# Performance work log

Hardware: AMD Instinct MI355X
Metric: run time of the kernel (lower is better)

## Reference

```python
import jax, jax.numpy as jnp
import numpy as np

S, B, C = 7, 2, 20
L_OBJ, L_NOBJ = 5.0, 0.5
EPS = 1e-06


def setup_inputs() -> dict:
    key = jax.random.key(0)
    k1, k2, k3 = jax.random.split(key, 3)
    N = 16384
    pred = jax.random.normal(k1, (N, S, S, B * 5 + C), dtype=jnp.float32)
    tgt = jax.random.uniform(k2, (N, S, S, 5 + C), dtype=jnp.float32)
    # objectness flag must be exactly 0.0 or 1.0 (loss tests true_box[0] == 1)
    obj = (jax.random.uniform(k3, (N, S, S)) < 0.3).astype(jnp.float32)
    target = tgt.at[..., 0].set(obj)
    return {"pred": pred, "target": target}


def _iou(cx1, cy1, w1, h1, cx2, cy2, w2, h2):
    # center-format boxes -> IoU (broadcasts over trailing B dim)
    b1x1, b1y1, b1x2, b1y2 = cx1 - w1 / 2, cy1 - h1 / 2, cx1 + w1 / 2, cy1 + h1 / 2
    b2x1, b2y1, b2x2, b2y2 = cx2 - w2 / 2, cy2 - h2 / 2, cx2 + w2 / 2, cy2 + h2 / 2
    iw = jnp.clip(jnp.minimum(b1x2, b2x2) - jnp.maximum(b1x1, b2x1), 0.0)
    ih = jnp.clip(jnp.minimum(b1y2, b2y2) - jnp.maximum(b1y1, b2y1), 0.0)
    inter = iw * ih
    a1 = (b1x2 - b1x1) * (b1y2 - b1y1)
    a2 = (b2x2 - b2x1) * (b2y2 - b2y1)
    return inter / (a1 + a2 - inter + EPS)


def _yolo_loss(pred, target):
    N = pred.shape[0]
    pb = pred[..., : B * 5].reshape(N, S, S, B, 5)          # [N,S,S,B,5]
    pcls = pred[..., B * 5:]                                 # [N,S,S,C]
    tconf = target[..., 0]                                   # [N,S,S]
    tx, ty, tw, th = target[..., 1], target[..., 2], target[..., 3], target[..., 4]
    tcls = target[..., 5:]                                   # [N,S,S,C]

    i_idx = jnp.arange(S, dtype=pred.dtype)[None, :, None]   # row index i
    j_idx = jnp.arange(S, dtype=pred.dtype)[None, None, :]   # col index j

    # absolute pred boxes [N,S,S,B]
    p_conf = pb[..., 0]
    p_x = (j_idx[..., None] + pb[..., 1]) / S
    p_y = (i_idx[..., None] + pb[..., 2]) / S
    p_w = jax.nn.relu(pb[..., 3])
    p_h = jax.nn.relu(pb[..., 4])

    # absolute true box [N,S,S,1] for broadcast vs B
    t_x = ((j_idx + tx) / S)[..., None]
    t_y = ((i_idx + ty) / S)[..., None]
    t_w_raw = tw[..., None]
    t_h_raw = th[..., None]

    # obj branch: true box with raw w/h ; noobj branch: relu'd (is_pred=True)
    iou_obj = _iou(p_x, p_y, p_w, p_h, t_x, t_y, t_w_raw, t_h_raw)            # [N,S,S,B]
    iou_no = _iou(p_x, p_y, p_w, p_h, t_x, t_y, jax.nn.relu(t_w_raw), jax.nn.relu(t_h_raw))

    def gather_best(arr, idx):
        return jnp.take_along_axis(arr, idx[..., None], axis=-1)[..., 0]

    # ---- object cells ----
    best_o = jnp.argmax(iou_obj, axis=-1)                    # [N,S,S]
    bx = gather_best(pb[..., 1], best_o)
    by = gather_best(pb[..., 2], best_o)
    bw = jax.nn.relu(gather_best(pb[..., 3], best_o))
    bh = jax.nn.relu(gather_best(pb[..., 4], best_o))
    bconf_o = gather_best(p_conf, best_o)
    biou = jax.lax.stop_gradient(gather_best(iou_obj, best_o))

    xy_loss = (bx - tx) ** 2 + (by - ty) ** 2
    wh_loss = (jnp.sqrt(jnp.abs(bw + EPS)) - jnp.sqrt(jnp.abs(tw + EPS))) ** 2 + \
              (jnp.sqrt(jnp.abs(bh + EPS)) - jnp.sqrt(jnp.abs(th + EPS))) ** 2
    conf_obj = (jax.nn.sigmoid(bconf_o) - biou) ** 2
    class_loss = jnp.sum((jax.nn.softmax(pcls, axis=-1) - tcls) ** 2, axis=-1)
    loss_obj = L_OBJ * (xy_loss + wh_loss) + conf_obj + class_loss

    # ---- no-object cells ----
    best_n = jnp.argmax(iou_no, axis=-1)
    bconf_n = gather_best(p_conf, best_n)
    loss_noobj = L_NOBJ * jax.nn.sigmoid(bconf_n) ** 2

    obj_mask = tconf == 1.0
    total = jnp.sum(jnp.where(obj_mask, loss_obj, loss_noobj))
    return total / N


def reference(pred, target):
    return _yolo_loss(pred, target)
```

## Files before the change

### kernel.cpp

```cpp
#include <hip/hip_runtime.h>

#define SS 7
#define NB 2
#define NC 20
#define PRED_W (NB * 5 + NC)
#define TGT_W  (5 + NC)
#define BLOCK  256

constexpr float L_OBJ  = 5.0f;
constexpr float L_NOBJ = 0.5f;
constexpr float EPSV   = 1e-6f;

__device__ __forceinline__ float sigmoidf_(float x) {
    return 1.0f / (1.0f + expf(-x));
}

__device__ __forceinline__ float iou_(float cx1, float cy1, float w1, float h1,
                                      float cx2, float cy2, float w2, float h2) {
    float b1x1 = cx1 - w1 * 0.5f, b1y1 = cy1 - h1 * 0.5f;
    float b1x2 = cx1 + w1 * 0.5f, b1y2 = cy1 + h1 * 0.5f;
    float b2x1 = cx2 - w2 * 0.5f, b2y1 = cy2 - h2 * 0.5f;
    float b2x2 = cx2 + w2 * 0.5f, b2y2 = cy2 + h2 * 0.5f;
    float iw = fmaxf(fminf(b1x2, b2x2) - fmaxf(b1x1, b2x1), 0.0f);
    float ih = fmaxf(fminf(b1y2, b2y2) - fmaxf(b1y1, b2y1), 0.0f);
    float inter = iw * ih;
    float a1 = (b1x2 - b1x1) * (b1y2 - b1y1);
    float a2 = (b2x2 - b2x1) * (b2y2 - b2y1);
    return inter / (a1 + a2 - inter + EPSV);
}

__global__ void zero_out_kernel(float* out) {
    out[0] = 0.0f;
}

__global__ __launch_bounds__(BLOCK) void yolo_loss_kernel(
        const float* __restrict__ pred,
        const float* __restrict__ target,
        float* __restrict__ out,
        float inv_n) {
    __shared__ float predS[BLOCK * PRED_W];
    __shared__ float tgtS[BLOCK * TGT_W];

    const int block0 = blockIdx.x * BLOCK;

    {
        const float4* pg = reinterpret_cast<const float4*>(pred + (size_t)block0 * PRED_W);
        float4* ps = reinterpret_cast<float4*>(predS);
        #pragma unroll
        for (int idx = threadIdx.x; idx < BLOCK * PRED_W / 4; idx += BLOCK)
            ps[idx] = pg[idx];
        const float4* tg = reinterpret_cast<const float4*>(target + (size_t)block0 * TGT_W);
        float4* ts = reinterpret_cast<float4*>(tgtS);
        #pragma unroll
        for (int idx = threadIdx.x; idx < BLOCK * TGT_W / 4; idx += BLOCK)
            ts[idx] = tg[idx];
    }
    __syncthreads();

    const int c    = threadIdx.x;
    const int cell = block0 + c;
    const int ij   = cell % (SS * SS);
    const int i    = ij / SS;
    const int j    = ij % SS;

    float p[PRED_W];
    {
        const float2* pr = reinterpret_cast<const float2*>(predS + c * PRED_W);
        #pragma unroll
        for (int k = 0; k < PRED_W / 2; ++k) {
            float2 v = pr[k];
            p[2 * k]     = v.x;
            p[2 * k + 1] = v.y;
        }
    }
    float t[TGT_W];
    {
        const float* tr = tgtS + c * TGT_W;
        #pragma unroll
        for (int k = 0; k < TGT_W; ++k) t[k] = tr[k];
    }

    const float tconf = t[0];
    const float tx = t[1], ty = t[2], tw = t[3], th = t[4];

    const float fi = (float)i, fj = (float)j;
    const float invS = 1.0f / (float)SS;

    const float t_x = (fj + tx) * invS;
    const float t_y = (fi + ty) * invS;

    float iou_b[NB];
    #pragma unroll
    for (int b = 0; b < NB; ++b) {
        float px = (fj + p[b * 5 + 1]) * invS;
        float py = (fi + p[b * 5 + 2]) * invS;
        float pw = fmaxf(p[b * 5 + 3], 0.0f);
        float ph = fmaxf(p[b * 5 + 4], 0.0f);
        iou_b[b] = iou_(px, py, pw, ph, t_x, t_y, tw, th);
    }

    const int best = (iou_b[1] > iou_b[0]) ? 1 : 0;

    const float bconf = p[best * 5 + 0];
    const float bx    = p[best * 5 + 1];
    const float by    = p[best * 5 + 2];
    const float bw    = fmaxf(p[best * 5 + 3], 0.0f);
    const float bh    = fmaxf(p[best * 5 + 4], 0.0f);
    const float biou  = iou_b[best];

    const float dx = bx - tx, dy = by - ty;
    const float xy_loss = dx * dx + dy * dy;

    const float sw = sqrtf(fabsf(bw + EPSV)) - sqrtf(fabsf(tw + EPSV));
    const float sh = sqrtf(fabsf(bh + EPSV)) - sqrtf(fabsf(th + EPSV));
    const float wh_loss = sw * sw + sh * sh;

    const float dc = sigmoidf_(bconf) - biou;
    const float conf_obj = dc * dc;

    float m = p[NB * 5];
    #pragma unroll
    for (int k = 1; k < NC; ++k) m = fmaxf(m, p[NB * 5 + k]);
    float esum = 0.0f;
    float e[NC];
    #pragma unroll
    for (int k = 0; k < NC; ++k) {
        e[k] = expf(p[NB * 5 + k] - m);
        esum += e[k];
    }
    const float inv_esum = 1.0f / esum;
    float class_loss = 0.0f;
    #pragma unroll
    for (int k = 0; k < NC; ++k) {
        float d = e[k] * inv_esum - t[5 + k];
        class_loss += d * d;
    }

    const float loss_obj = L_OBJ * (xy_loss + wh_loss) + conf_obj + class_loss;

    const float sn = sigmoidf_(bconf);
    const float loss_noobj = L_NOBJ * sn * sn;

    float loss = (tconf == 1.0f) ? loss_obj : loss_noobj;

    #pragma unroll
    for (int off = 32; off > 0; off >>= 1)
        loss += __shfl_down(loss, off, 64);

    __shared__ float wsum[BLOCK / 64];
    const int lane = threadIdx.x & 63;
    const int wid  = threadIdx.x >> 6;
    if (lane == 0) wsum[wid] = loss;
    __syncthreads();
    if (threadIdx.x == 0) {
        float s = wsum[0] + wsum[1] + wsum[2] + wsum[3];
        atomicAdd(out, s * inv_n);
    }
}

extern "C" void kernel_launch(void* const* d_in, const int* in_sizes, int n_in,
                              void* d_out, int out_size, void* d_ws, size_t ws_size,
                              hipStream_t stream) {
    const float* pred   = (const float*)d_in[0];
    const float* target = (const float*)d_in[1];
    float* out = (float*)d_out;

    int n = in_sizes[0] / (SS * SS * PRED_W);
    int ncells = n * SS * SS;
    float inv_n = 1.0f / (float)n;

    zero_out_kernel<<<1, 1, 0, stream>>>(out);

    int grid = ncells / BLOCK;
    yolo_loss_kernel<<<grid, BLOCK, 0, stream>>>(pred, target, out, inv_n);
}
```

Baseline: 217.3 us.

## Load tiles per wave via direct global-to-LDS DMA and use fast exp

Replaces the block-wide float4 copy into shared memory and the block barrier with per-wave global_load_lds DMA transfers, so each wave waits only on its own vmcnt before reading its 64 cells. Target values are read directly from LDS instead of being copied into a register array. expf is swapped for __expf in the sigmoid and softmax. The per-wave LDS layout hard-codes offsets for 30/25-float rows, and the fast exp slightly changes numerics.

```diff
diff --git a/kernel.cpp b/kernel.cpp
--- a/kernel.cpp
+++ b/kernel.cpp
@@ -3,16 +3,28 @@
 #define SS 7
 #define NB 2
 #define NC 20
-#define PRED_W (NB * 5 + NC)
-#define TGT_W  (5 + NC)
+#define PRED_W 30
+#define TGT_W  25
 #define BLOCK  256
+#define WPB    (BLOCK / 64)
 
 constexpr float L_OBJ  = 5.0f;
 constexpr float L_NOBJ = 0.5f;
 constexpr float EPSV   = 1e-6f;
 
+__device__ __forceinline__ void dma16(const float* g, float* s) {
+    __builtin_amdgcn_global_load_lds(
+        (const __attribute__((address_space(1))) unsigned int*)g,
+        (__attribute__((address_space(3))) unsigned int*)s, 16, 0, 0);
+}
+__device__ __forceinline__ void dma4(const float* g, float* s) {
+    __builtin_amdgcn_global_load_lds(
+        (const __attribute__((address_space(1))) unsigned int*)g,
+        (__attribute__((address_space(3))) unsigned int*)s, 4, 0, 0);
+}
+
 __device__ __forceinline__ float sigmoidf_(float x) {
-    return 1.0f / (1.0f + expf(-x));
+    return 1.0f / (1.0f + __expf(-x));
 }
 
 __device__ __forceinline__ float iou_(float cx1, float cy1, float w1, float h1,
@@ -38,34 +50,40 @@
         const float* __restrict__ target,
         float* __restrict__ out,
         float inv_n) {
-    __shared__ float predS[BLOCK * PRED_W];
-    __shared__ float tgtS[BLOCK * TGT_W];
+    __shared__ float predS[WPB * 64 * PRED_W];
+    __shared__ float tgtS [WPB * 64 * TGT_W];
 
-    const int block0 = blockIdx.x * BLOCK;
+    const int wave = threadIdx.x >> 6;
+    const int lane = threadIdx.x & 63;
+    const int cell0 = blockIdx.x * BLOCK + wave * 64;
 
-    {
-        const float4* pg = reinterpret_cast<const float4*>(pred + (size_t)block0 * PRED_W);
-        float4* ps = reinterpret_cast<float4*>(predS);
-        #pragma unroll
-        for (int idx = threadIdx.x; idx < BLOCK * PRED_W / 4; idx += BLOCK)
-            ps[idx] = pg[idx];
-        const float4* tg = reinterpret_cast<const float4*>(target + (size_t)block0 * TGT_W);
-        float4* ts = reinterpret_cast<float4*>(tgtS);
-        #pragma unroll
-        for (int idx = threadIdx.x; idx < BLOCK * TGT_W / 4; idx += BLOCK)
-            ts[idx] = tg[idx];
-    }
-    __syncthreads();
+    const float* gp = pred   + (size_t)cell0 * PRED_W;
+    const float* gt = target + (size_t)cell0 * TGT_W;
+    float* sp = predS + wave * (64 * PRED_W);
+    float* st = tgtS  + wave * (64 * TGT_W);
 
-    const int c    = threadIdx.x;
-    const int cell = block0 + c;
-    const int ij   = cell % (SS * SS);
-    const int i    = ij / SS;
-    const int j    = ij % SS;
+    #pragma unroll
+    for (int k = 0; k < 7; ++k)
+        dma16(gp + k * 256 + lane * 4, sp + k * 256);
+    #pragma unroll
+    for (int r = 0; r < 2; ++r)
+        dma4(gp + 1792 + r * 64 + lane, sp + 1792 + r * 64);
+
+    #pragma unroll
+    for (int k = 0; k < 6; ++k)
+        dma16(gt + k * 256 + lane * 4, st + k * 256);
+    dma4(gt + 1536 + lane, st + 1536);
+
+    asm volatile("s_waitcnt vmcnt(0)" ::: "memory");
+
+    const int cell = cell0 + lane;
+    const int ij = cell % (SS * SS);
+    const int i  = ij / SS;
+    const int j  = ij % SS;
 
     float p[PRED_W];
     {
-        const float2* pr = reinterpret_cast<const float2*>(predS + c * PRED_W);
+        const float2* pr = reinterpret_cast<const float2*>(sp + lane * PRED_W);
         #pragma unroll
         for (int k = 0; k < PRED_W / 2; ++k) {
             float2 v = pr[k];
@@ -73,15 +91,9 @@
             p[2 * k + 1] = v.y;
         }
     }
-    float t[TGT_W];
-    {
-        const float* tr = tgtS + c * TGT_W;
-        #pragma unroll
-        for (int k = 0; k < TGT_W; ++k) t[k] = tr[k];
-    }
-
-    const float tconf = t[0];
-    const float tx = t[1], ty = t[2], tw = t[3], th = t[4];
+    const float* tr = st + lane * TGT_W;
+    const float tconf = tr[0];
+    const float tx = tr[1], ty = tr[2], tw = tr[3], th = tr[4];
 
     const float fi = (float)i, fj = (float)j;
     const float invS = 1.0f / (float)SS;
@@ -125,14 +137,14 @@
     float e[NC];
     #pragma unroll
     for (int k = 0; k < NC; ++k) {
-        e[k] = expf(p[NB * 5 + k] - m);
+        e[k] = __expf(p[NB * 5 + k] - m);
         esum += e[k];
     }
     const float inv_esum = 1.0f / esum;
     float class_loss = 0.0f;
     #pragma unroll
     for (int k = 0; k < NC; ++k) {
-        float d = e[k] * inv_esum - t[5 + k];
+        float d = e[k] * inv_esum - tr[5 + k];
         class_loss += d * d;
     }
 
@@ -147,10 +159,8 @@
     for (int off = 32; off > 0; off >>= 1)
         loss += __shfl_down(loss, off, 64);
 
-    __shared__ float wsum[BLOCK / 64];
-    const int lane = threadIdx.x & 63;
-    const int wid  = threadIdx.x >> 6;
-    if (lane == 0) wsum[wid] = loss;
+    __shared__ float wsum[WPB];
+    if (lane == 0) wsum[wave] = loss;
     __syncthreads();
     if (threadIdx.x == 0) {
         float s = wsum[0] + wsum[1] + wsum[2] + wsum[3];
```

After: 196.6 us. 1.11x faster.
